# Kernel tuning notes

Measured on AMD Instinct MI355X. Metric: run time of the kernel, lower is better.

## Reference

```python
import jax, jax.numpy as jnp
import numpy as np

TAU = 1.0

def setup_inputs() -> dict:
    key = jax.random.key(0)
    k1, k2 = jax.random.split(key)
    b, t, n, e, top_k = 2, 64, 1024, 512, 256
    x = jax.random.normal(k1, (b, t, n, e), dtype=jnp.float32)
    # torch nn.Linear(embed_size, top_k): weight [top_k, e], bias [top_k]
    W = jax.random.normal(k2, (top_k, e), dtype=jnp.float32) * (1.0 / np.sqrt(e))
    b_bias = jnp.zeros((top_k,), dtype=jnp.float32)
    return {"x": x, "W": W, "b_bias": b_bias}

def reference(x, W, b_bias):
    b, t, n, e = x.shape
    x_flat = x.reshape(b, t * n, e)                 # [b, m, e], m = t*n
    scores = x_flat @ W.T + b_bias                  # [b, m, top_k]
    weights = jax.nn.softmax(scores / TAU, axis=1)  # softmax over token axis m
    # weighted-sum pooling for all top_k slots at once (replaces torch loop)
    selected = jnp.einsum('bmk,bme->bke', weights, x_flat)  # [b, top_k, e]
    return selected
```

## Files before the change

kernel.cpp:

```cpp
#include <hip/hip_runtime.h>
#include <stdint.h>

#define B_DIM 2
#define M_DIM 65536
#define E_DIM 512
#define K_DIM 256

typedef __bf16 bf16_t;
typedef __bf16 bf16x8 __attribute__((ext_vector_type(8)));
typedef float  f32x4  __attribute__((ext_vector_type(4)));
typedef float  f32x16 __attribute__((ext_vector_type(16)));
typedef int    i32x8  __attribute__((ext_vector_type(8)));

typedef const __attribute__((address_space(1))) void* gas_ptr;
typedef __attribute__((address_space(3))) void* las_ptr;

__device__ __forceinline__ void async_load16(const void* g, void* l) {
    __builtin_amdgcn_global_load_lds((gas_ptr)g, (las_ptr)l, 16, 0, 0);
}

__device__ __forceinline__ unsigned short bf16_bits(float f) {
    return __builtin_bit_cast(unsigned short, (__bf16)f);
}
__device__ __forceinline__ unsigned int pack2(float lo, float hi) {
    return (unsigned int)bf16_bits(lo) | ((unsigned int)bf16_bits(hi) << 16);
}
__device__ __forceinline__ float bf16u_to_f32(unsigned short us) {
    return __builtin_bit_cast(float, (unsigned)us << 16);
}
__device__ __forceinline__ uint2 pack8_fp8(const float* f) {
    int lo = __builtin_amdgcn_cvt_pk_fp8_f32(f[0], f[1], 0, false);
    lo = __builtin_amdgcn_cvt_pk_fp8_f32(f[2], f[3], lo, true);
    int hi = __builtin_amdgcn_cvt_pk_fp8_f32(f[4], f[5], 0, false);
    hi = __builtin_amdgcn_cvt_pk_fp8_f32(f[6], f[7], hi, true);
    return make_uint2((unsigned)lo, (unsigned)hi);
}

__global__ __launch_bounds__(256) void cast_w(const float* __restrict__ W, bf16_t* __restrict__ Wb) {
    int idx = blockIdx.x * 256 + threadIdx.x;
    float4 v = ((const float4*)W)[idx];
    ((uint2*)Wb)[idx] = make_uint2(pack2(v.x, v.y), pack2(v.z, v.w));
}

__global__ __launch_bounds__(256) void gemm1_exp_t(const float* __restrict__ x, const bf16_t* __restrict__ Wb,
                                                   unsigned char* __restrict__ pb8, float* __restrict__ psums,
                                                   unsigned char* __restrict__ xT8) {
    int gid = blockIdx.x;
    int mt = gid & 1023;
    int b  = gid >> 10;
    int m0 = mt * 64;
    int t = threadIdx.x, lane = t & 63, w = t >> 6;

    __shared__ __align__(16) char smem[40960];
    bf16_t* Alds = (bf16_t*)smem;
    bf16_t* Blds = (bf16_t*)(smem + 32768);
    bf16_t* Elds = (bf16_t*)smem;

    const float* xb = x + ((size_t)b * M_DIM + m0) * E_DIM;

    f32x4 zero = {0.f, 0.f, 0.f, 0.f};
    f32x4 acc[4][4];
#pragma unroll
    for (int i = 0; i < 4; ++i)
#pragma unroll
        for (int j = 0; j < 4; ++j) acc[i][j] = zero;

    int bst_r = t >> 2, bst_s0 = t & 3;

    int q = lane >> 4, r15 = lane & 15;

    for (int ke = 0; ke < 8; ++ke) {
        int e0 = ke * 64;
#pragma unroll
        for (int is = 0; is < 8; ++is) {
            int c = is * 256 + t;
            int row = c >> 3, sl = c & 7;
            int ge = sl ^ (row & 7);
            async_load16(Wb + (size_t)row * E_DIM + e0 + ge * 8, Alds + c * 8);
        }
#pragma unroll
        for (int sg = 0; sg < 2; ++sg) {
            int sl = bst_s0 + sg * 4;
            int ge = sl ^ (bst_r & 7);
            const float4* f = (const float4*)(xb + (size_t)bst_r * E_DIM + e0 + ge * 8);
            float4 a0 = f[0], a1 = f[1];
            *(uint4*)(Blds + bst_r * 64 + sl * 8) =
                make_uint4(pack2(a0.x, a0.y), pack2(a0.z, a0.w), pack2(a1.x, a1.y), pack2(a1.z, a1.w));
        }
        __syncthreads();

#pragma unroll
        for (int h = 0; h < 2; ++h) {
            bf16x8 af[4], bfr[4];
#pragma unroll
            for (int i = 0; i < 4; ++i) {
                int r = w * 64 + i * 16 + r15;
                int sl = (h * 4 + q) ^ (r & 7);
                af[i] = *(const bf16x8*)(Alds + r * 64 + sl * 8);
            }
#pragma unroll
            for (int j = 0; j < 4; ++j) {
                int r = j * 16 + r15;
                int sl = (h * 4 + q) ^ (r & 7);
                bfr[j] = *(const bf16x8*)(Blds + r * 64 + sl * 8);
            }
#pragma unroll
            for (int i = 0; i < 4; ++i)
#pragma unroll
                for (int j = 0; j < 4; ++j)
                    acc[i][j] = __builtin_amdgcn_mfma_f32_16x16x32_bf16(af[i], bfr[j], acc[i][j], 0, 0, 0);
        }

        {
            const unsigned short* Bs = (const unsigned short*)Blds;
            int l7 = t & 7;
            int mbase = l7 * 8;
            int ebase = t >> 3;
#pragma unroll
            for (int p = 0; p < 2; ++p) {
                int ecol = p * 32 + ebase;
                float f[8];
#pragma unroll
                for (int s = 0; s < 8; ++s) {
                    int mmr = (s + l7) & 7;
                    int sl = (ecol >> 3) ^ mmr;
                    f[mmr] = bf16u_to_f32(Bs[(mbase + mmr) * 64 + sl * 8 + (ecol & 7)]);
                }
                *(uint2*)(xT8 + ((size_t)(b * E_DIM + e0 + ecol)) * M_DIM + m0 + mbase) = pack8_fp8(f);
            }
        }
        __syncthreads();
    }

    int cc = lane & 15;
    float ksum[4][4];
#pragma unroll
    for (int i = 0; i < 4; ++i)
#pragma unroll
        for (int p = 0; p < 4; ++p) ksum[i][p] = 0.f;

#pragma unroll
    for (int i = 0; i < 4; ++i) {
        int kr = w * 64 + i * 16 + q * 4;
#pragma unroll
        for (int j = 0; j < 4; ++j) {
            int colb = j * 16 + cc;
            int g = colb >> 3, off = colb & 7;
#pragma unroll
            for (int p = 0; p < 4; ++p) {
                float v = __expf(acc[i][j][p]);
                ksum[i][p] += v;
                int k = kr + p;
                Elds[k * 64 + ((g ^ (k & 7)) * 8) + off] = (bf16_t)v;
            }
        }
    }
#pragma unroll
    for (int mask = 1; mask < 16; mask <<= 1)
#pragma unroll
        for (int i = 0; i < 4; ++i)
#pragma unroll
            for (int p = 0; p < 4; ++p)
                ksum[i][p] += __shfl_xor(ksum[i][p], mask, 64);
    if (cc == 0) {
        float* pp = psums + (size_t)b * K_DIM * 1024 + mt;
#pragma unroll
        for (int i = 0; i < 4; ++i)
#pragma unroll
            for (int p = 0; p < 4; ++p)
                pp[(size_t)(w * 64 + i * 16 + q * 4 + p) * 1024] = ksum[i][p];
    }
    __syncthreads();

    {
        int g = t & 7, rsub = t >> 3;
        unsigned char* dstb = pb8 + (size_t)b * K_DIM * M_DIM + m0;
#pragma unroll
        for (int p = 0; p < 8; ++p) {
            int k = p * 32 + rsub;
            const unsigned short* src = (const unsigned short*)(Elds + k * 64 + ((g ^ (k & 7)) * 8));
            float f[8];
#pragma unroll
            for (int s = 0; s < 8; ++s) f[s] = bf16u_to_f32(src[s]);
            *(uint2*)(dstb + (size_t)k * M_DIM + g * 8) = pack8_fp8(f);
        }
    }
}

__global__ __launch_bounds__(256) void gemm2(const unsigned char* __restrict__ pb8, const unsigned char* __restrict__ xT8,
                                             float* __restrict__ part) {
    int p_ = blockIdx.x;
    int xcd = p_ & 7, idx = p_ >> 3;
    int kt_et = idx & 7, cb = idx >> 3;
    int kt = kt_et & 1, et = kt_et >> 1;
    int c2 = (cb << 3) | xcd;
    int ch = c2 & 31, b = c2 >> 5;
    int lbid = kt | (et << 1) | (ch << 3) | (b << 8);

    int t = threadIdx.x, lane = t & 63, w = t >> 6;
    int wk = w & 1, we = w >> 1;

    __shared__ __align__(16) unsigned char Alds[2][128 * 64];
    __shared__ __align__(16) unsigned char Blds[2][128 * 64];

    const unsigned char* Ab = pb8 + ((size_t)(b * K_DIM + kt * 128)) * M_DIM + ch * 2048;
    const unsigned char* Bb = xT8 + ((size_t)(b * E_DIM + et * 128)) * M_DIM + ch * 2048;

    f32x16 acc[2][2];
#pragma unroll
    for (int i = 0; i < 2; ++i)
#pragma unroll
        for (int j = 0; j < 2; ++j)
#pragma unroll
            for (int p = 0; p < 16; ++p) acc[i][j][p] = 0.f;

    int l31 = lane & 31, g = lane >> 5;

    auto STAGE = [&](int buf, int m0) {
#pragma unroll
        for (int is = 0; is < 2; ++is) {
            int c = is * 256 + t;
            int row = c >> 2, a = c & 3;
            int sr = (row & 3) ^ ((row >> 2) & 3);
            int bsl = a ^ sr;
            async_load16(Ab + (size_t)row * M_DIM + m0 + bsl * 16, &Alds[buf][c * 16]);
            async_load16(Bb + (size_t)row * M_DIM + m0 + bsl * 16, &Blds[buf][c * 16]);
        }
    };

    STAGE(0, 0);
    __syncthreads();

    for (int km = 0; km < 32; ++km) {
        int cur = km & 1;
        if (km + 1 < 32) STAGE(cur ^ 1, (km + 1) * 64);

        i32x8 av[2], bv[2];
#pragma unroll
        for (int i = 0; i < 2; ++i) {
            int r = wk * 64 + i * 32 + l31;
            int sr = (r & 3) ^ ((r >> 2) & 3);
            int4 lo = *(const int4*)(&Alds[cur][r * 64 + (((2 * g) ^ sr) * 16)]);
            int4 hi = *(const int4*)(&Alds[cur][r * 64 + (((2 * g + 1) ^ sr) * 16)]);
            av[i][0] = lo.x; av[i][1] = lo.y; av[i][2] = lo.z; av[i][3] = lo.w;
            av[i][4] = hi.x; av[i][5] = hi.y; av[i][6] = hi.z; av[i][7] = hi.w;
        }
#pragma unroll
        for (int j = 0; j < 2; ++j) {
            int r = we * 64 + j * 32 + l31;
            int sr = (r & 3) ^ ((r >> 2) & 3);
            int4 lo = *(const int4*)(&Blds[cur][r * 64 + (((2 * g) ^ sr) * 16)]);
            int4 hi = *(const int4*)(&Blds[cur][r * 64 + (((2 * g + 1) ^ sr) * 16)]);
            bv[j][0] = lo.x; bv[j][1] = lo.y; bv[j][2] = lo.z; bv[j][3] = lo.w;
            bv[j][4] = hi.x; bv[j][5] = hi.y; bv[j][6] = hi.z; bv[j][7] = hi.w;
        }

        __builtin_amdgcn_s_setprio(1);
#pragma unroll
        for (int i = 0; i < 2; ++i)
#pragma unroll
            for (int j = 0; j < 2; ++j)
                acc[i][j] = __builtin_amdgcn_mfma_scale_f32_32x32x64_f8f6f4(
                    av[i], bv[j], acc[i][j],
                    0 , 0 ,
                    0, 0x7f7f7f7f ,
                    0, 0x7f7f7f7f );
        __builtin_amdgcn_s_setprio(0);

        __syncthreads();
    }

    float* pp = part + (size_t)lbid * 16384;
#pragma unroll
    for (int i = 0; i < 2; ++i)
#pragma unroll
        for (int p = 0; p < 16; ++p) {
            int kl = wk * 64 + i * 32 + (p & 3) + 8 * (p >> 2) + 4 * g;
#pragma unroll
            for (int j = 0; j < 2; ++j) {
                int el = we * 64 + j * 32 + l31;
                pp[kl * 128 + el] = acc[i][j][p];
            }
        }
}

__global__ __launch_bounds__(256) void reduce_out(const float* __restrict__ part, const float* __restrict__ psums,
                                                  float* __restrict__ out) {
    int bid = blockIdx.x;
    int ehalf = bid & 1, k = (bid >> 1) & 255, b = bid >> 9;
    int t = threadIdx.x, lane = t & 63;

    const float* ps = psums + (size_t)b * K_DIM * 1024 + (size_t)k * 1024;
    float cs = 0.f;
#pragma unroll
    for (int c = 0; c < 4; ++c) cs += ps[c * 256 + t];
#pragma unroll
    for (int mask = 1; mask < 64; mask <<= 1) cs += __shfl_xor(cs, mask, 64);
    __shared__ float cspart[4];
    if (lane == 0) cspart[t >> 6] = cs;
    __syncthreads();
    float colsum = (cspart[0] + cspart[1]) + (cspart[2] + cspart[3]);

    int e = ehalf * 256 + t;
    int kt = k >> 7, kl = k & 127, et = e >> 7, el = e & 127;
    float s = 0.f;
#pragma unroll
    for (int ch = 0; ch < 32; ++ch) {
        int bid2 = kt | (et << 1) | (ch << 3) | (b << 8);
        s += part[(size_t)bid2 * 16384 + kl * 128 + el];
    }
    out[((size_t)(b * 256 + k)) * 512 + e] = s / colsum;
}

extern "C" void kernel_launch(void* const* d_in, const int* in_sizes, int n_in,
                              void* d_out, int out_size, void* d_ws, size_t ws_size,
                              hipStream_t stream) {
    (void)in_sizes; (void)n_in; (void)out_size; (void)ws_size;
    const float* x = (const float*)d_in[0];
    const float* W = (const float*)d_in[1];

    char* ws = (char*)d_ws;
    unsigned char* xT8 = (unsigned char*)ws;
    bf16_t* Wb    = (bf16_t*)(ws + 67108864);
    unsigned char* pb8 = (unsigned char*)(ws + 67371008);
    float*  psums = (float*)(ws + 100925440);
    float*  part  = (float*)(ws + 103022592);
    float*  out   = (float*)d_out;

    cast_w<<<128, 256, 0, stream>>>(W, Wb);
    gemm1_exp_t<<<2048, 256, 0, stream>>>(x, Wb, pb8, psums, xT8);
    gemm2<<<512, 256, 0, stream>>>(pb8, xT8, part);
    reduce_out<<<1024, 256, 0, stream>>>(part, psums, out);
}
```

Baseline: 436.0 us.

## Double-buffer W and x tiles in gemm1 to overlap loads with MFMA

Converts the gemm1 K-loop into a double-buffered pipeline. The next W tile is async-loaded into the alternate LDS buffer and the next x slice is prefetched into registers while MFMAs run on the current buffer, which also removes one barrier per iteration. LDS grows from 40KB to 80KB, and launch bounds request 2 blocks per CU. That may cap occupancy and adds register pressure for the prefetched x values. A possible hazard is the missing trailing sync: Elds aliases smem later, and the xT8 transpose reads Bl while other waves may already be writing.

```diff
diff --git a/kernel.cpp b/kernel.cpp
--- a/kernel.cpp
+++ b/kernel.cpp
@@ -42,18 +42,16 @@
     ((uint2*)Wb)[idx] = make_uint2(pack2(v.x, v.y), pack2(v.z, v.w));
 }
 
-__global__ __launch_bounds__(256) void gemm1_exp_t(const float* __restrict__ x, const bf16_t* __restrict__ Wb,
-                                                   unsigned char* __restrict__ pb8, float* __restrict__ psums,
-                                                   unsigned char* __restrict__ xT8) {
+__global__ __launch_bounds__(256, 2) void gemm1_exp_t(const float* __restrict__ x, const bf16_t* __restrict__ Wb,
+                                                      unsigned char* __restrict__ pb8, float* __restrict__ psums,
+                                                      unsigned char* __restrict__ xT8) {
     int gid = blockIdx.x;
     int mt = gid & 1023;
     int b  = gid >> 10;
     int m0 = mt * 64;
     int t = threadIdx.x, lane = t & 63, w = t >> 6;
 
-    __shared__ __align__(16) char smem[40960];
-    bf16_t* Alds = (bf16_t*)smem;
-    bf16_t* Blds = (bf16_t*)(smem + 32768);
+    __shared__ __align__(16) char smem[81920];
     bf16_t* Elds = (bf16_t*)smem;
 
     const float* xb = x + ((size_t)b * M_DIM + m0) * E_DIM;
@@ -66,28 +64,56 @@
         for (int j = 0; j < 4; ++j) acc[i][j] = zero;
 
     int bst_r = t >> 2, bst_s0 = t & 3;
+    int ge0 = bst_s0 ^ (bst_r & 7);
+    int ge1 = (bst_s0 + 4) ^ (bst_r & 7);
 
     int q = lane >> 4, r15 = lane & 15;
 
-    for (int ke = 0; ke < 8; ++ke) {
-        int e0 = ke * 64;
+    float4 xr0, xr1, xr2, xr3;
+    {
+        const float4* f0 = (const float4*)(xb + (size_t)bst_r * E_DIM + ge0 * 8);
+        const float4* f1 = (const float4*)(xb + (size_t)bst_r * E_DIM + ge1 * 8);
+        xr0 = f0[0]; xr1 = f0[1];
+        xr2 = f1[0]; xr3 = f1[1];
+    }
+    {
+        bf16_t* Al = (bf16_t*)smem;
 #pragma unroll
         for (int is = 0; is < 8; ++is) {
             int c = is * 256 + t;
             int row = c >> 3, sl = c & 7;
             int ge = sl ^ (row & 7);
-            async_load16(Wb + (size_t)row * E_DIM + e0 + ge * 8, Alds + c * 8);
-        }
-#pragma unroll
-        for (int sg = 0; sg < 2; ++sg) {
-            int sl = bst_s0 + sg * 4;
-            int ge = sl ^ (bst_r & 7);
-            const float4* f = (const float4*)(xb + (size_t)bst_r * E_DIM + e0 + ge * 8);
-            float4 a0 = f[0], a1 = f[1];
-            *(uint4*)(Blds + bst_r * 64 + sl * 8) =
-                make_uint4(pack2(a0.x, a0.y), pack2(a0.z, a0.w), pack2(a1.x, a1.y), pack2(a1.z, a1.w));
-        }
+            async_load16(Wb + (size_t)row * E_DIM + 0 + ge * 8, Al + c * 8);
+        }
+    }
+
+    for (int ke = 0; ke < 8; ++ke) {
+        int e0 = ke * 64;
+        int cur = ke & 1;
+        bf16_t* Al = (bf16_t*)(smem + cur * 32768);
+        bf16_t* Bl = (bf16_t*)(smem + 65536 + cur * 8192);
+
+        *(uint4*)(Bl + bst_r * 64 + bst_s0 * 8) =
+            make_uint4(pack2(xr0.x, xr0.y), pack2(xr0.z, xr0.w), pack2(xr1.x, xr1.y), pack2(xr1.z, xr1.w));
+        *(uint4*)(Bl + bst_r * 64 + (bst_s0 + 4) * 8) =
+            make_uint4(pack2(xr2.x, xr2.y), pack2(xr2.z, xr2.w), pack2(xr3.x, xr3.y), pack2(xr3.z, xr3.w));
+
         __syncthreads();
+
+        if (ke < 7) {
+            bf16_t* An = (bf16_t*)(smem + (cur ^ 1) * 32768);
+#pragma unroll
+            for (int is = 0; is < 8; ++is) {
+                int c = is * 256 + t;
+                int row = c >> 3, sl = c & 7;
+                int ge = sl ^ (row & 7);
+                async_load16(Wb + (size_t)row * E_DIM + (e0 + 64) + ge * 8, An + c * 8);
+            }
+            const float4* f0 = (const float4*)(xb + (size_t)bst_r * E_DIM + (e0 + 64) + ge0 * 8);
+            const float4* f1 = (const float4*)(xb + (size_t)bst_r * E_DIM + (e0 + 64) + ge1 * 8);
+            xr0 = f0[0]; xr1 = f0[1];
+            xr2 = f1[0]; xr3 = f1[1];
+        }
 
 #pragma unroll
         for (int h = 0; h < 2; ++h) {
@@ -96,13 +122,13 @@
             for (int i = 0; i < 4; ++i) {
                 int r = w * 64 + i * 16 + r15;
                 int sl = (h * 4 + q) ^ (r & 7);
-                af[i] = *(const bf16x8*)(Alds + r * 64 + sl * 8);
+                af[i] = *(const bf16x8*)(Al + r * 64 + sl * 8);
             }
 #pragma unroll
             for (int j = 0; j < 4; ++j) {
                 int r = j * 16 + r15;
                 int sl = (h * 4 + q) ^ (r & 7);
-                bfr[j] = *(const bf16x8*)(Blds + r * 64 + sl * 8);
+                bfr[j] = *(const bf16x8*)(Bl + r * 64 + sl * 8);
             }
 #pragma unroll
             for (int i = 0; i < 4; ++i)
@@ -112,7 +138,7 @@
         }
 
         {
-            const unsigned short* Bs = (const unsigned short*)Blds;
+            const unsigned short* Bs = (const unsigned short*)Bl;
             int l7 = t & 7;
             int mbase = l7 * 8;
             int ebase = t >> 3;
@@ -129,7 +155,6 @@
                 *(uint2*)(xT8 + ((size_t)(b * E_DIM + e0 + ecol)) * M_DIM + m0 + mbase) = pack8_fp8(f);
             }
         }
-        __syncthreads();
     }
 
     int cc = lane & 15;
```

Result: no change. 434.5 us (-0.4%).
